# Kernel tuning notes

Measured on AMD Instinct MI355X. Metric: run time of the kernel, lower is better.

## Reference

```python
import jax, jax.numpy as jnp
import numpy as np

N_HEADS = 16
ROPE_BASE = 10000.0


def _apply_rope(t, cos, sin):
    # t: (B, H, S, D); cos/sin: (S, D/2). Rotate-half convention.
    d2 = t.shape[-1] // 2
    t1, t2 = t[..., :d2], t[..., d2:]
    return jnp.concatenate([t1 * cos - t2 * sin, t2 * cos + t1 * sin], axis=-1)


def setup_inputs() -> dict:
    key = jax.random.key(0)
    k0, k1, k2, k3, k4 = jax.random.split(key, 5)
    B, S, E = 4, 2048, 1024
    scale = 0.02
    x = jax.random.normal(k0, (B, S, E), dtype=jnp.float32)
    w_qkv = jax.random.normal(k1, (E, 3 * E), dtype=jnp.float32) * scale
    b_qkv = jnp.zeros((3 * E,), dtype=jnp.float32)
    w_proj = jax.random.normal(k2, (E, E), dtype=jnp.float32) * scale
    b_proj = jnp.zeros((E,), dtype=jnp.float32)
    return {"x": x, "w_qkv": w_qkv, "b_qkv": b_qkv, "w_proj": w_proj, "b_proj": b_proj}


def reference(x, w_qkv, b_qkv, w_proj, b_proj):
    B, S, E = x.shape
    H = N_HEADS
    D = E // H
    # fused QKV projection
    qkv = x @ w_qkv + b_qkv                      # (B, S, 3E)
    q, k, v = jnp.split(qkv, 3, axis=-1)
    def to_heads(t):
        return t.reshape(B, S, H, D).transpose(0, 2, 1, 3)  # (B, H, S, D)
    q, k, v = to_heads(q), to_heads(k), to_heads(v)
    # RoPE (rotate-half)
    inv_freq = ROPE_BASE ** (-jnp.arange(0, D, 2, dtype=jnp.float32) / D)  # (D/2,)
    pos = jnp.arange(S, dtype=jnp.float32)
    freqs = pos[:, None] * inv_freq[None, :]     # (S, D/2)
    cos, sin = jnp.cos(freqs), jnp.sin(freqs)
    q = _apply_rope(q, cos, sin)
    k = _apply_rope(k, cos, sin)
    # causal SDPA
    scores = jnp.einsum('bhqd,bhkd->bhqk', q, k) / jnp.sqrt(jnp.float32(D))
    causal = jnp.tril(jnp.ones((S, S), dtype=bool))
    scores = jnp.where(causal, scores, jnp.float32(-1e30))
    probs = jax.nn.softmax(scores, axis=-1)
    out = jnp.einsum('bhqk,bhkd->bhqd', probs, v)  # (B, H, S, D)
    out = out.transpose(0, 2, 1, 3).reshape(B, S, E)
    # output projection (dropout is identity at p=0 / eval)
    return out @ w_proj + b_proj
```

## Files before the change

### kernel.cpp

```cpp
#include <hip/hip_runtime.h>

typedef unsigned short u16;
typedef __bf16 bf16x8 __attribute__((ext_vector_type(8)));
typedef float f32x4 __attribute__((ext_vector_type(4)));

__device__ __forceinline__ u16 f2b(float f) {
    unsigned u = __builtin_bit_cast(unsigned, f);
    unsigned r = (u + 0x7fffu + ((u >> 16) & 1u)) >> 16;
    return (u16)r;
}
#if __has_builtin(__builtin_amdgcn_cvt_pk_bf16_f32)
typedef __bf16 bf16x2_t __attribute__((ext_vector_type(2)));
__device__ __forceinline__ unsigned pk2(float a, float b) {
    return __builtin_bit_cast(unsigned, __builtin_amdgcn_cvt_pk_bf16_f32(a, b));
}
#else
__device__ __forceinline__ unsigned pk2(float a, float b) {
    return (unsigned)f2b(a) | ((unsigned)f2b(b) << 16);
}
#endif
#if __has_builtin(__builtin_amdgcn_exp2f)
#define EXP2F(x) __builtin_amdgcn_exp2f(x)
#else
#define EXP2F(x) exp2f(x)
#endif

__device__ __forceinline__ void gl_lds16(const u16* g, u16* l) {
    __builtin_amdgcn_global_load_lds(
        (const __attribute__((address_space(1))) unsigned*)(const void*)g,
        (__attribute__((address_space(3))) unsigned*)(void*)l, 16, 0, 0);
}

__device__ __forceinline__ void transpose64(const float* __restrict__ in,
                                            u16* __restrict__ out, int R, int C,
                                            int tr, int tc, int tid, u16 (*tile)[72]) {
    for (int i = tid; i < 4096; i += 256) {
        int r = i >> 6, c = i & 63;
        tile[c][r] = f2b(in[(size_t)(tr + r) * C + tc + c]);
    }
    __syncthreads();
    for (int i = tid; i < 4096; i += 256) {
        int r = i >> 6, c = i & 63;
        out[(size_t)(tc + r) * R + tr + c] = tile[r][c];
    }
}

__global__ __launch_bounds__(256) void k_prep(const float* __restrict__ x,
                                              u16* __restrict__ x_bf,
                                              const float* __restrict__ w_qkv,
                                              u16* __restrict__ wqkvT,
                                              const float* __restrict__ w_proj,
                                              u16* __restrict__ wprojT,
                                              float2* __restrict__ tab) {
    __shared__ u16 tile[64][72];
    int bid = blockIdx.x, tid = threadIdx.x;
    if (bid < 4096) {
        int i = bid * 256 + tid;
        const float4* p = (const float4*)(x + (size_t)i * 8);
        float4 a = p[0], b = p[1];
        u16 t[8] = {f2b(a.x), f2b(a.y), f2b(a.z), f2b(a.w),
                    f2b(b.x), f2b(b.y), f2b(b.z), f2b(b.w)};
        *(uint4*)(x_bf + (size_t)i * 8) = *(const uint4*)t;
    } else if (bid < 4864) {
        int q = bid - 4096;
        transpose64(w_qkv, wqkvT, 1024, 3072, (q / 48) * 64, (q % 48) * 64, tid, tile);
    } else if (bid < 5120) {
        int q = bid - 4864;
        transpose64(w_proj, wprojT, 1024, 1024, (q / 16) * 64, (q % 16) * 64, tid, tile);
    } else {
        int i = (bid - 5120) * 256 + tid;
        int s = i >> 5, d = i & 31;
        const float C0 = 0.4152410118609203f;
        float inv_freq = exp2f(-C0 * (float)d);
        float sn, cs;
        sincosf((float)s * inv_freq, &sn, &cs);
        tab[i] = make_float2(cs, sn);
    }
}

__device__ __forceinline__ void gemm_mainloop(const u16* __restrict__ Ab,
                                              const u16* __restrict__ Bb, int K,
                                              u16* As, u16* Bs, int tid,
                                              f32x4 (&acc)[4][4]) {
    const int wave = tid >> 6, lane = tid & 63;
    const int col = lane & 15, quad = lane >> 4;
    const int wm = wave >> 1, wn = wave & 1;
    const int lrow = lane >> 2, lk = (lane & 3) * 8;
    u16* ldsA0 = As + (wave * 16) * 32;
    u16* ldsA1 = As + (64 + wave * 16) * 32;
    u16* ldsB0 = Bs + (wave * 16) * 32;
    u16* ldsB1 = Bs + (64 + wave * 16) * 32;
    const u16* gA0 = Ab + (size_t)(wave * 16 + lrow) * K + lk;
    const u16* gA1 = gA0 + (size_t)64 * K;
    const u16* gB0 = Bb + (size_t)(wave * 16 + lrow) * K + lk;
    const u16* gB1 = gB0 + (size_t)64 * K;
    for (int k0 = 0; k0 < K; k0 += 64) {
        if (k0) __syncthreads();
#pragma unroll
        for (int kh = 0; kh < 2; ++kh) {
            int ko = k0 + kh * 32;
            gl_lds16(gA0 + ko, ldsA0 + kh * 4096);
            gl_lds16(gA1 + ko, ldsA1 + kh * 4096);
            gl_lds16(gB0 + ko, ldsB0 + kh * 4096);
            gl_lds16(gB1 + ko, ldsB1 + kh * 4096);
        }
        __syncthreads();
#pragma unroll
        for (int kh = 0; kh < 2; ++kh) {
            bf16x8 af[4], bfr[4];
#pragma unroll
            for (int mt = 0; mt < 4; ++mt)
                af[mt] = *(const bf16x8*)(As + kh * 4096 +
                                          (wm * 64 + mt * 16 + col) * 32 + quad * 8);
#pragma unroll
            for (int nt = 0; nt < 4; ++nt)
                bfr[nt] = *(const bf16x8*)(Bs + kh * 4096 +
                                           (wn * 64 + nt * 16 + col) * 32 + quad * 8);
#pragma unroll
            for (int mt = 0; mt < 4; ++mt)
#pragma unroll
                for (int nt = 0; nt < 4; ++nt)
                    acc[mt][nt] = __builtin_amdgcn_mfma_f32_16x16x32_bf16(
                        af[mt], bfr[nt], acc[mt][nt], 0, 0, 0);
        }
    }
}

__global__ __launch_bounds__(256) void k_gemm_qkv_rope(
    const u16* __restrict__ A, const u16* __restrict__ Bt,
    const float* __restrict__ bias, const float2* __restrict__ tab,
    u16* __restrict__ Qr, u16* __restrict__ Kr, u16* __restrict__ Vt) {
    __shared__ __align__(16) u16 smem[16384];
    u16* As = smem;
    u16* Bs = smem + 8192;
    const int K = 1024;
    int tid = threadIdx.x;
    int lane = tid & 63, wave = tid >> 6;
    int col = lane & 15, quad = lane >> 4;
    int wm = wave >> 1, wn = wave & 1;
    int mBase = blockIdx.y * 128;
    int nBase = blockIdx.x * 128;
    f32x4 acc[4][4] = {};
    gemm_mainloop(A + (size_t)mBase * K, Bt + (size_t)nBase * K, K, As, Bs, tid, acc);

    int region = nBase >> 10;
    int n64 = nBase + wn * 64;
    int h = (n64 & 1023) >> 6;
    if (region < 2) {
        __syncthreads();
        float qs = (region == 0) ? 0.18033688011112042f : 1.0f;
#pragma unroll
        for (int nt = 0; nt < 2; ++nt) {
            int d1 = nt * 16 + col;
            float b1 = bias[n64 + d1];
            float b2 = bias[n64 + d1 + 32];
            int nl = wn * 64 + nt * 16 + col;
#pragma unroll
            for (int mt = 0; mt < 4; ++mt) {
                int mlb = wm * 64 + mt * 16 + quad * 4;
#pragma unroll
                for (int r = 0; r < 4; ++r) {
                    int mloc = mlb + r;
                    int s = (mBase + mloc) & 2047;
                    float2 t = tab[s * 32 + d1];
                    float t1 = acc[mt][nt][r] + b1;
                    float t2 = acc[mt][nt + 2][r] + b2;
                    int sw = (mloc & 7) << 3;
                    smem[mloc * 128 + (nl ^ sw)] = f2b((t1 * t.x - t2 * t.y) * qs);
                    smem[mloc * 128 + ((nl + 32) ^ sw)] = f2b((t2 * t.x + t1 * t.y) * qs);
                }
            }
        }
        __syncthreads();
        u16* outp = (region == 0) ? Qr : Kr;
#pragma unroll
        for (int p = 0; p < 8; ++p) {
            int lin = p * 256 + tid;
            int mloc = lin >> 4;
            int c8 = (lin & 15) << 3;
            uint4 v = *(const uint4*)(smem + mloc * 128 + (c8 ^ ((mloc & 7) << 3)));
            int m = mBase + mloc;
            int s = m & 2047, b = m >> 11;
            int ng = (nBase & 1023) + c8;
            *(uint4*)(outp + ((size_t)((b * 16 + (ng >> 6)) * 2048 + s)) * 64 +
                      (ng & 63)) = v;
        }
    } else {
        int b = mBase >> 11;
        int sb0 = mBase & 2047;
#pragma unroll
        for (int nt = 0; nt < 4; ++nt) {
            int d = nt * 16 + col;
            float bv = bias[n64 + d];
            u16* vrow = Vt + ((size_t)((b * 16 + h) * 64 + d)) * 2048;
#pragma unroll
            for (int mt = 0; mt < 4; ++mt) {
                int s = sb0 + wm * 64 + mt * 16 + quad * 4;
                uint2 w;
                w.x = pk2(acc[mt][nt][0] + bv, acc[mt][nt][1] + bv);
                w.y = pk2(acc[mt][nt][2] + bv, acc[mt][nt][3] + bv);
                *(uint2*)(vrow + s) = w;
            }
        }
    }
}

__device__ __forceinline__ void stage_kv(const u16* __restrict__ Kt,
                                         const u16* __restrict__ Vtb, u16* KsB,
                                         u16* VsB, int wave, int lane) {
    int lr = lane >> 3;
    int lc = lane & 7;
#pragma unroll
    for (int i = 0; i < 2; ++i) {
        int s = wave * 2 + i;
        int r = s * 8 + lr;
        int key = (r & 3) | (((r >> 3) & 1) << 2);
        gl_lds16(Kt + (size_t)r * 64 + ((lc ^ key) << 3), KsB + s * 512);
    }
#pragma unroll
    for (int i = 0; i < 2; ++i) {
        int s = wave * 2 + i;
        int d = s * 8 + lr;
        int key = d & 7;
        gl_lds16(Vtb + (size_t)d * 2048 + ((lc ^ key) << 3), VsB + s * 512);
    }
}

__global__ __launch_bounds__(256, 4) void k_attn(const u16* __restrict__ Qr,
                                                 const u16* __restrict__ Kr,
                                                 const u16* __restrict__ Vt,
                                                 u16* __restrict__ O) {
    __shared__ __align__(16) u16 Ks[2][4096];
    __shared__ __align__(16) u16 Vs[2][4096];
    int tid = threadIdx.x, wave = tid >> 6, lane = tid & 63;
    int col = lane & 15, quad = lane >> 4;
    int id = blockIdx.x + (blockIdx.y << 4);
    int xcd = id & 7, w = id >> 3;
    int head = xcd * 8 + (w & 7);
    int tsel = w >> 3;
    int b = head >> 4, h = head & 15;
    size_t headQ = (size_t)head * 2048 * 64;
    size_t headV = (size_t)head * 64 * 2048;
    int prow = (col >> 2) * 8 + (col & 3);
    int ck = col & 7;

#pragma unroll 1
    for (int phase = 0; phase < 2; ++phase) {
        int T = phase ? tsel : 31 - tsel;
        int myq = T * 64 + wave * 16 + col;
        const u16* qp = Qr + headQ + (size_t)myq * 64;
        bf16x8 aq0 = *(const bf16x8*)(qp + quad * 8);
        bf16x8 aq1 = *(const bf16x8*)(qp + 32 + quad * 8);
        f32x4 o[4] = {};
        float l = 0.f;

        stage_kv(Kr + headQ, Vt + headV, Ks[0], Vs[0], wave, lane);
        __syncthreads();

        for (int j = 0; j <= T; ++j) {
            int cur = j & 1;
            if (j < T)
                stage_kv(Kr + headQ + ((size_t)(j + 1) << 12),
                         Vt + headV + (j + 1) * 64, Ks[cur ^ 1], Vs[cur ^ 1],
                         wave, lane);
            const u16* KsC = Ks[cur];
            const u16* VsC = Vs[cur];
            f32x4 s[4];
            __builtin_amdgcn_s_setprio(1);
#pragma unroll
            for (int nt = 0; nt < 4; ++nt) {
                const u16* kp = KsC + ((nt & 1) * 32 + (nt >> 1) * 4 + prow) * 64;
                bf16x8 ak0 = *(const bf16x8*)(kp + ((quad ^ ck) << 3));
                bf16x8 ak1 = *(const bf16x8*)(kp + (((quad + 4) ^ ck) << 3));
                f32x4 z = {};
                z = __builtin_amdgcn_mfma_f32_16x16x32_bf16(ak0, aq0, z, 0, 0, 0);
                s[nt] = __builtin_amdgcn_mfma_f32_16x16x32_bf16(ak1, aq1, z, 0, 0, 0);
            }
            __builtin_amdgcn_s_setprio(0);
            if (j == T) {
#pragma unroll
                for (int nt = 0; nt < 4; ++nt) {
                    int keyb = j * 64 + (nt & 1) * 32 + quad * 8 + (nt >> 1) * 4;
#pragma unroll
                    for (int r = 0; r < 4; ++r)
                        if (keyb + r > myq) s[nt][r] = -3.0e38f;
                }
            }
            unsigned P4[8];
#pragma unroll
            for (int nt = 0; nt < 4; ++nt) {
                float p0 = EXP2F(s[nt][0]);
                float p1 = EXP2F(s[nt][1]);
                float p2 = EXP2F(s[nt][2]);
                float p3 = EXP2F(s[nt][3]);
                l += (p0 + p1) + (p2 + p3);
                P4[2 * nt] = pk2(p0, p1);
                P4[2 * nt + 1] = pk2(p2, p3);
            }
            __builtin_amdgcn_s_setprio(1);
#pragma unroll
            for (int kk = 0; kk < 2; ++kk) {
                uint4 bw;
                bw.x = P4[2 * kk];
                bw.y = P4[2 * kk + 1];
                bw.z = P4[2 * kk + 4];
                bw.w = P4[2 * kk + 5];
                bf16x8 bp = __builtin_bit_cast(bf16x8, bw);
#pragma unroll
                for (int mt = 0; mt < 4; ++mt) {
                    bf16x8 av = *(const bf16x8*)(VsC + (mt * 16 + col) * 64 +
                                                 (((kk * 4 + quad) ^ ck) << 3));
                    o[mt] = __builtin_amdgcn_mfma_f32_16x16x32_bf16(av, bp, o[mt], 0, 0, 0);
                }
            }
            __builtin_amdgcn_s_setprio(0);
            __syncthreads();
        }
        l += __shfl_xor(l, 16);
        l += __shfl_xor(l, 32);
        float inv = 1.0f / l;
        u16* orow = O + (size_t)(b * 2048 + myq) * 1024 + h * 64;
#pragma unroll
        for (int mt = 0; mt < 4; ++mt) {
            uint2 w2;
            w2.x = pk2(o[mt][0] * inv, o[mt][1] * inv);
            w2.y = pk2(o[mt][2] * inv, o[mt][3] * inv);
            *(uint2*)(orow + mt * 16 + quad * 4) = w2;
        }
    }
}

__device__ __forceinline__ void proj_mainloop(const u16* __restrict__ Ab,
                                              const u16* __restrict__ Bb,
                                              u16* As, u16* Bs, int tid,
                                              f32x4 (&acc)[2][4]) {
    const int wave = tid >> 6, lane = tid & 63;
    const int col = lane & 15, quad = lane >> 4;
    const int lrow = lane >> 2, lk = (lane & 3) * 8;
    u16* ldsA0 = As + (wave * 16) * 32;
    u16* ldsA1 = As + (64 + wave * 16) * 32;
    u16* ldsB0 = Bs + (wave * 16) * 32;
    const u16* gA0 = Ab + (size_t)(wave * 16 + lrow) * 1024 + lk;
    const u16* gA1 = gA0 + (size_t)64 * 1024;
    const u16* gB0 = Bb + (size_t)(wave * 16 + lrow) * 1024 + lk;
    for (int k0 = 0; k0 < 1024; k0 += 64) {
        if (k0) __syncthreads();
#pragma unroll
        for (int kh = 0; kh < 2; ++kh) {
            int ko = k0 + kh * 32;
            gl_lds16(gA0 + ko, ldsA0 + kh * 4096);
            gl_lds16(gA1 + ko, ldsA1 + kh * 4096);
            gl_lds16(gB0 + ko, ldsB0 + kh * 2048);
        }
        __syncthreads();
#pragma unroll
        for (int kh = 0; kh < 2; ++kh) {
            bf16x8 af[2], bfr[4];
#pragma unroll
            for (int mt = 0; mt < 2; ++mt)
                af[mt] = *(const bf16x8*)(As + kh * 4096 +
                                          (wave * 32 + mt * 16 + col) * 32 + quad * 8);
#pragma unroll
            for (int nt = 0; nt < 4; ++nt)
                bfr[nt] = *(const bf16x8*)(Bs + kh * 2048 +
                                           (nt * 16 + col) * 32 + quad * 8);
#pragma unroll
            for (int mt = 0; mt < 2; ++mt)
#pragma unroll
                for (int nt = 0; nt < 4; ++nt)
                    acc[mt][nt] = __builtin_amdgcn_mfma_f32_16x16x32_bf16(
                        af[mt], bfr[nt], acc[mt][nt], 0, 0, 0);
        }
    }
}

__global__ __launch_bounds__(256, 4) void k_gemm_proj(const u16* __restrict__ A,
                                                      const u16* __restrict__ Bt,
                                                      const float* __restrict__ bias,
                                                      float* __restrict__ out) {
    __shared__ __align__(16) u16 As[2 * 128 * 32];
    __shared__ __align__(16) u16 Bs[2 * 64 * 32];
    int tid = threadIdx.x;
    int lane = tid & 63, wave = tid >> 6;
    int col = lane & 15, quad = lane >> 4;
    int mBase = blockIdx.y * 128;
    int nBase = blockIdx.x * 64;
    f32x4 acc[2][4] = {};
    proj_mainloop(A + (size_t)mBase * 1024, Bt + (size_t)nBase * 1024, As, Bs, tid, acc);
#pragma unroll
    for (int nt = 0; nt < 4; ++nt) {
        int n = nBase + nt * 16 + col;
        float bv = bias[n];
#pragma unroll
        for (int mt = 0; mt < 2; ++mt) {
            int m = mBase + wave * 32 + mt * 16 + quad * 4;
#pragma unroll
            for (int r = 0; r < 4; ++r)
                out[(size_t)(m + r) * 1024 + n] = acc[mt][nt][r] + bv;
        }
    }
}

extern "C" void kernel_launch(void* const* d_in, const int* in_sizes, int n_in,
                              void* d_out, int out_size, void* d_ws, size_t ws_size,
                              hipStream_t stream) {
    const float* x = (const float*)d_in[0];
    const float* w_qkv = (const float*)d_in[1];
    const float* b_qkv = (const float*)d_in[2];
    const float* w_proj = (const float*)d_in[3];
    const float* b_proj = (const float*)d_in[4];
    float* out = (float*)d_out;
    char* ws = (char*)d_ws;
    u16* x_bf = (u16*)(ws);
    u16* wqkvT = (u16*)(ws + 16777216);
    u16* wprojT = (u16*)(ws + 23068672);
    u16* Qr = (u16*)(ws + 25165824);
    u16* Kr = (u16*)(ws + 41943040);
    u16* Vt = (u16*)(ws + 58720256);
    u16* AO = (u16*)(ws + 75497472);
    float2* tab = (float2*)(ws + 75497472);

    k_prep<<<5376, 256, 0, stream>>>(x, x_bf, w_qkv, wqkvT, w_proj, wprojT, tab);
    k_gemm_qkv_rope<<<dim3(24, 64), 256, 0, stream>>>(x_bf, wqkvT, b_qkv, tab, Qr, Kr, Vt);
    k_attn<<<dim3(16, 64), 256, 0, stream>>>(Qr, Kr, Vt, AO);
    k_gemm_proj<<<dim3(16, 64), 256, 0, stream>>>(AO, wprojT, b_proj, out);
}
```

Before: 252.2 us.

## Fuse both causal query-tile phases into one KV sweep sharing K/V loads

Measured after the change: 251.7 us. About the same (-0.2%).

```diff
diff --git a/kernel.cpp b/kernel.cpp
--- a/kernel.cpp
+++ b/kernel.cpp
@@ -244,89 +244,133 @@
     int prow = (col >> 2) * 8 + (col & 3);
     int ck = col & 7;
 
-#pragma unroll 1
-    for (int phase = 0; phase < 2; ++phase) {
-        int T = phase ? tsel : 31 - tsel;
-        int myq = T * 64 + wave * 16 + col;
-        const u16* qp = Qr + headQ + (size_t)myq * 64;
-        bf16x8 aq0 = *(const bf16x8*)(qp + quad * 8);
-        bf16x8 aq1 = *(const bf16x8*)(qp + 32 + quad * 8);
-        f32x4 o[4] = {};
-        float l = 0.f;
-
-        stage_kv(Kr + headQ, Vt + headV, Ks[0], Vs[0], wave, lane);
-        __syncthreads();
-
-        for (int j = 0; j <= T; ++j) {
-            int cur = j & 1;
-            if (j < T)
-                stage_kv(Kr + headQ + ((size_t)(j + 1) << 12),
-                         Vt + headV + (j + 1) * 64, Ks[cur ^ 1], Vs[cur ^ 1],
-                         wave, lane);
-            const u16* KsC = Ks[cur];
-            const u16* VsC = Vs[cur];
-            f32x4 s[4];
-            __builtin_amdgcn_s_setprio(1);
+    int T0 = 31 - tsel;
+    int T1 = tsel;
+    int myq0 = T0 * 64 + wave * 16 + col;
+    int myq1 = T1 * 64 + wave * 16 + col;
+    const u16* qp0 = Qr + headQ + (size_t)myq0 * 64;
+    const u16* qp1 = Qr + headQ + (size_t)myq1 * 64;
+    bf16x8 aq00 = *(const bf16x8*)(qp0 + quad * 8);
+    bf16x8 aq01 = *(const bf16x8*)(qp0 + 32 + quad * 8);
+    bf16x8 aq10 = *(const bf16x8*)(qp1 + quad * 8);
+    bf16x8 aq11 = *(const bf16x8*)(qp1 + 32 + quad * 8);
+    f32x4 o0[4] = {}, o1[4] = {};
+    float l0 = 0.f, l1 = 0.f;
+
+    stage_kv(Kr + headQ, Vt + headV, Ks[0], Vs[0], wave, lane);
+    __syncthreads();
+
+    for (int j = 0; j <= T0; ++j) {
+        int cur = j & 1;
+        if (j < T0)
+            stage_kv(Kr + headQ + ((size_t)(j + 1) << 12), Vt + headV + (j + 1) * 64,
+                     Ks[cur ^ 1], Vs[cur ^ 1], wave, lane);
+        bool d1 = (j <= T1);
+        const u16* KsC = Ks[cur];
+        const u16* VsC = Vs[cur];
+        f32x4 s0[4], s1[4];
+        __builtin_amdgcn_s_setprio(1);
+#pragma unroll
+        for (int nt = 0; nt < 4; ++nt) {
+            const u16* kp = KsC + ((nt & 1) * 32 + (nt >> 1) * 4 + prow) * 64;
+            bf16x8 ak0 = *(const bf16x8*)(kp + ((quad ^ ck) << 3));
+            bf16x8 ak1 = *(const bf16x8*)(kp + (((quad + 4) ^ ck) << 3));
+            {
+                f32x4 z = {};
+                z = __builtin_amdgcn_mfma_f32_16x16x32_bf16(ak0, aq00, z, 0, 0, 0);
+                s0[nt] = __builtin_amdgcn_mfma_f32_16x16x32_bf16(ak1, aq01, z, 0, 0, 0);
+            }
+            if (d1) {
+                f32x4 z = {};
+                z = __builtin_amdgcn_mfma_f32_16x16x32_bf16(ak0, aq10, z, 0, 0, 0);
+                s1[nt] = __builtin_amdgcn_mfma_f32_16x16x32_bf16(ak1, aq11, z, 0, 0, 0);
+            }
+        }
+        __builtin_amdgcn_s_setprio(0);
+        if (j == T0) {
 #pragma unroll
             for (int nt = 0; nt < 4; ++nt) {
-                const u16* kp = KsC + ((nt & 1) * 32 + (nt >> 1) * 4 + prow) * 64;
-                bf16x8 ak0 = *(const bf16x8*)(kp + ((quad ^ ck) << 3));
-                bf16x8 ak1 = *(const bf16x8*)(kp + (((quad + 4) ^ ck) << 3));
-                f32x4 z = {};
-                z = __builtin_amdgcn_mfma_f32_16x16x32_bf16(ak0, aq0, z, 0, 0, 0);
-                s[nt] = __builtin_amdgcn_mfma_f32_16x16x32_bf16(ak1, aq1, z, 0, 0, 0);
-            }
-            __builtin_amdgcn_s_setprio(0);
-            if (j == T) {
-#pragma unroll
-                for (int nt = 0; nt < 4; ++nt) {
-                    int keyb = j * 64 + (nt & 1) * 32 + quad * 8 + (nt >> 1) * 4;
-#pragma unroll
-                    for (int r = 0; r < 4; ++r)
-                        if (keyb + r > myq) s[nt][r] = -3.0e38f;
-                }
-            }
-            unsigned P4[8];
+                int keyb = j * 64 + (nt & 1) * 32 + quad * 8 + (nt >> 1) * 4;
+#pragma unroll
+                for (int r = 0; r < 4; ++r)
+                    if (keyb + r > myq0) s0[nt][r] = -3.0e38f;
+            }
+        }
+        if (j == T1) {
 #pragma unroll
             for (int nt = 0; nt < 4; ++nt) {
-                float p0 = EXP2F(s[nt][0]);
-                float p1 = EXP2F(s[nt][1]);
-                float p2 = EXP2F(s[nt][2]);
-                float p3 = EXP2F(s[nt][3]);
-                l += (p0 + p1) + (p2 + p3);
-                P4[2 * nt] = pk2(p0, p1);
-                P4[2 * nt + 1] = pk2(p2, p3);
-            }
-            __builtin_amdgcn_s_setprio(1);
-#pragma unroll
-            for (int kk = 0; kk < 2; ++kk) {
-                uint4 bw;
-                bw.x = P4[2 * kk];
-                bw.y = P4[2 * kk + 1];
-                bw.z = P4[2 * kk + 4];
-                bw.w = P4[2 * kk + 5];
-                bf16x8 bp = __builtin_bit_cast(bf16x8, bw);
-#pragma unroll
-                for (int mt = 0; mt < 4; ++mt) {
-                    bf16x8 av = *(const bf16x8*)(VsC + (mt * 16 + col) * 64 +
-                                                 (((kk * 4 + quad) ^ ck) << 3));
-                    o[mt] = __builtin_amdgcn_mfma_f32_16x16x32_bf16(av, bp, o[mt], 0, 0, 0);
-                }
-            }
-            __builtin_amdgcn_s_setprio(0);
-            __syncthreads();
-        }
-        l += __shfl_xor(l, 16);
-        l += __shfl_xor(l, 32);
-        float inv = 1.0f / l;
-        u16* orow = O + (size_t)(b * 2048 + myq) * 1024 + h * 64;
-#pragma unroll
-        for (int mt = 0; mt < 4; ++mt) {
-            uint2 w2;
-            w2.x = pk2(o[mt][0] * inv, o[mt][1] * inv);
-            w2.y = pk2(o[mt][2] * inv, o[mt][3] * inv);
-            *(uint2*)(orow + mt * 16 + quad * 4) = w2;
-        }
+                int keyb = j * 64 + (nt & 1) * 32 + quad * 8 + (nt >> 1) * 4;
+#pragma unroll
+                for (int r = 0; r < 4; ++r)
+                    if (keyb + r > myq1) s1[nt][r] = -3.0e38f;
+            }
+        }
+        unsigned P40[8], P41[8];
+#pragma unroll
+        for (int nt = 0; nt < 4; ++nt) {
+            float p0 = EXP2F(s0[nt][0]);
+            float p1 = EXP2F(s0[nt][1]);
+            float p2 = EXP2F(s0[nt][2]);
+            float p3 = EXP2F(s0[nt][3]);
+            l0 += (p0 + p1) + (p2 + p3);
+            P40[2 * nt] = pk2(p0, p1);
+            P40[2 * nt + 1] = pk2(p2, p3);
+        }
+        if (d1) {
+#pragma unroll
+            for (int nt = 0; nt < 4; ++nt) {
+                float p0 = EXP2F(s1[nt][0]);
+                float p1 = EXP2F(s1[nt][1]);
+                float p2 = EXP2F(s1[nt][2]);
+                float p3 = EXP2F(s1[nt][3]);
+                l1 += (p0 + p1) + (p2 + p3);
+                P41[2 * nt] = pk2(p0, p1);
+                P41[2 * nt + 1] = pk2(p2, p3);
+            }
+        }
+        __builtin_amdgcn_s_setprio(1);
+#pragma unroll
+        for (int kk = 0; kk < 2; ++kk) {
+            uint4 bw0;
+            bw0.x = P40[2 * kk];
+            bw0.y = P40[2 * kk + 1];
+            bw0.z = P40[2 * kk + 4];
+            bw0.w = P40[2 * kk + 5];
+            bf16x8 bp0 = __builtin_bit_cast(bf16x8, bw0);
+            uint4 bw1;
+            bw1.x = P41[2 * kk];
+            bw1.y = P41[2 * kk + 1];
+            bw1.z = P41[2 * kk + 4];
+            bw1.w = P41[2 * kk + 5];
+            bf16x8 bp1 = __builtin_bit_cast(bf16x8, bw1);
+#pragma unroll
+            for (int mt = 0; mt < 4; ++mt) {
+                bf16x8 av = *(const bf16x8*)(VsC + (mt * 16 + col) * 64 +
+                                             (((kk * 4 + quad) ^ ck) << 3));
+                o0[mt] = __builtin_amdgcn_mfma_f32_16x16x32_bf16(av, bp0, o0[mt], 0, 0, 0);
+                if (d1)
+                    o1[mt] = __builtin_amdgcn_mfma_f32_16x16x32_bf16(av, bp1, o1[mt], 0, 0, 0);
+            }
+        }
+        __builtin_amdgcn_s_setprio(0);
+        if (j < T0) __syncthreads();
+    }
+    l0 += __shfl_xor(l0, 16);
+    l0 += __shfl_xor(l0, 32);
+    l1 += __shfl_xor(l1, 16);
+    l1 += __shfl_xor(l1, 32);
+    float inv0 = 1.0f / l0, inv1 = 1.0f / l1;
+    u16* orow0 = O + (size_t)(b * 2048 + myq0) * 1024 + h * 64;
+    u16* orow1 = O + (size_t)(b * 2048 + myq1) * 1024 + h * 64;
+#pragma unroll
+    for (int mt = 0; mt < 4; ++mt) {
+        uint2 w0, w1;
+        w0.x = pk2(o0[mt][0] * inv0, o0[mt][1] * inv0);
+        w0.y = pk2(o0[mt][2] * inv0, o0[mt][3] * inv0);
+        w1.x = pk2(o1[mt][0] * inv1, o1[mt][1] * inv1);
+        w1.y = pk2(o1[mt][2] * inv1, o1[mt][3] * inv1);
+        *(uint2*)(orow0 + mt * 16 + quad * 4) = w0;
+        *(uint2*)(orow1 + mt * 16 + quad * 4) = w1;
     }
 }
 
```
